# Optimization experiments

Measured on AMD Instinct MI355X. Metric: run time of the kernel, lower is better.

## Reference

```python
import jax, jax.numpy as jnp
import numpy as np

V, A, E, K, F = 50000, 1000, 100, 256, 8   # vocab, num_apis, embed_dim, num_kernel, feature_dim
B, S = 256, 512                             # batch, seq_len
KS = (2, 3, 4, 5)


def setup_inputs() -> dict:
    key = jax.random.key(0)
    ks = jax.random.split(key, 32)
    rn = lambda k, shape, s=0.05: jax.random.normal(k, shape, dtype=jnp.float32) * s
    inp = {}
    inp["text_ids"] = jax.random.randint(ks[0], (B, S), 0, V)
    inp["emb_table"] = rn(ks[1], (V, E), 1.0).at[0].set(0.0)  # padding_idx=0
    for i, h in enumerate(KS):
        inp[f"conv_w{h}"] = rn(ks[2 + 2 * i], (K, E, h))
        inp[f"conv_b{h}"] = rn(ks[3 + 2 * i], (K,))
    inp["sc_fcl_w"] = rn(ks[10], (A, 4 * K)); inp["sc_fcl_b"] = rn(ks[11], (A,))
    inp["fic_fc_w"] = rn(ks[12], (F, 4 * K)); inp["fic_fc_b"] = rn(ks[13], (F,))
    inp["api_emb"] = jax.random.uniform(ks[14], (F, A), dtype=jnp.float32)  # nn.Parameter(torch.rand)
    inp["mlp_w1"] = rn(ks[15], (F, 2 * F)); inp["mlp_b1"] = rn(ks[16], (F,))
    inp["mlp_w2"] = rn(ks[17], (1, F));     inp["mlp_b2"] = rn(ks[18], (1,))
    inp["fic_fcl_w"] = rn(ks[19], (A, 2 * A)); inp["fic_fcl_b"] = rn(ks[20], (A,))
    inp["fusion_w"] = rn(ks[21], (A, 2 * A)); inp["fusion_b"] = rn(ks[22], (A,))
    inp["out_w"] = rn(ks[23], (A, A)); inp["out_b"] = rn(ks[24], (A,))
    return inp


def reference(text_ids, emb_table, conv_w2, conv_b2, conv_w3, conv_b3,
              conv_w4, conv_b4, conv_w5, conv_b5, sc_fcl_w, sc_fcl_b,
              fic_fc_w, fic_fc_b, api_emb, mlp_w1, mlp_b1, mlp_w2, mlp_b2,
              fic_fcl_w, fic_fcl_b, fusion_w, fusion_b, out_w, out_b):
    # Embedding -> [B, E, S] (channels-first for Conv1d)
    x = emb_table[text_ids].transpose(0, 2, 1)
    pooled = []
    for w, b in ((conv_w2, conv_b2), (conv_w3, conv_b3), (conv_w4, conv_b4), (conv_w5, conv_b5)):
        y = jax.lax.conv_general_dilated(x, w, (1,), 'VALID',
                                         dimension_numbers=('NCH', 'OIH', 'NCH'))
        y = jax.nn.relu(y + b[None, :, None])
        pooled.append(jnp.max(y, axis=-1))            # AdaptiveMaxPool1d(1)
    e = jnp.concatenate(pooled, axis=1)               # [B, 4K]
    u_sc = e @ sc_fcl_w.T + sc_fcl_b                  # [B, A]
    u_t = e @ fic_fc_w.T + fic_fc_b                   # [B, F]
    u_mm = u_t @ api_emb                              # [B, A]
    # Fused broadcast-MLP replacing the per-sample Python loop:
    # cat([u_t repeated over A, api_emb.T]) @ W1.T == u_t@W1a.T (+) apiT@W1b.T
    w1a, w1b = mlp_w1[:, :F], mlp_w1[:, F:]
    z = (u_t @ w1a.T)[:, None, :] + (api_emb.T @ w1b.T)[None, :, :] + mlp_b1  # [B, A, F]
    u_mlp = jnp.tanh(jnp.einsum('baf,f->ba', z, mlp_w2[0]) + mlp_b2[0])       # [B, A]
    u_fic = jnp.tanh(jnp.concatenate([u_mm, u_mlp], axis=1) @ fic_fcl_w.T + fic_fcl_b)
    u_mmf = jnp.concatenate([u_sc, u_fic], axis=1) @ fusion_w.T + fusion_b    # dropout = identity (eval)
    return u_mmf @ out_w.T + out_b
```

## Files before the change

kernel.cpp:

```cpp
#include <hip/hip_runtime.h>
#include <hip/hip_bf16.h>
#include <math.h>


typedef __attribute__((ext_vector_type(8))) short short8;
typedef __attribute__((ext_vector_type(4))) short short4v;
typedef __attribute__((ext_vector_type(4))) float f32x4;

__device__ __forceinline__ void gld_lds16(const void* g, void* l) {
  __builtin_amdgcn_global_load_lds(
      (const __attribute__((address_space(1))) unsigned int*)g,
      (__attribute__((address_space(3))) unsigned int*)l, 16, 0, 0);
}

__device__ __forceinline__ short bf16of(float f) {
  union { float f; unsigned u; } x; x.f = f;
  unsigned r = (x.u + 0x7fff + ((x.u >> 16) & 1)) >> 16;
  return (short)r;
}

#define O1 6400128
#define O2 7055488
#define O3 8104064
#define O4 10201216
#define O5 12298368
#define O6 13346944
#define OT 13478024
__global__ __launch_bounds__(256) void prep_all(
    const int* __restrict__ text_ids, const float* __restrict__ emb,
    const float* __restrict__ w2, const float* __restrict__ w3,
    const float* __restrict__ w4, const float* __restrict__ w5,
    const float* __restrict__ b2, const float* __restrict__ b3,
    const float* __restrict__ b4, const float* __restrict__ b5,
    const float* __restrict__ sc_w, const float* __restrict__ fic_w,
    const float* __restrict__ fus_w, const float* __restrict__ out_w,
    __hip_bfloat16* __restrict__ emb_bf, __hip_bfloat16* __restrict__ Wc,
    float* __restrict__ cb, __hip_bfloat16* __restrict__ wt_sc,
    __hip_bfloat16* __restrict__ wt_fic, __hip_bfloat16* __restrict__ wt_fus,
    __hip_bfloat16* __restrict__ wt_out, int* __restrict__ ids_pad) {
  for (int v = blockIdx.x * 256 + threadIdx.x; v < OT / 4;
       v += gridDim.x * 256) {
    const int idx = v * 4;
    if (idx < O1) {
      const int row = idx >> 7, e = idx & 127;
      float4 f = make_float4(0.f, 0.f, 0.f, 0.f);
      if (row < 50000 && e < 100)
        f = *(const float4*)(emb + row * 100 + e);
      *(short4v*)(emb_bf + idx) =
          (short4v){bf16of(f.x), bf16of(f.y), bf16of(f.z), bf16of(f.w)};
    } else if (idx < O2) {
      const int t = idx - O1;
      const int n = t / 640, k = t % 640;
      const int h = 2 + (n >> 8), kc = n & 255;
      const int dh = k >> 7, e = k & 127;
      const float* w = (h == 2) ? w2 : (h == 3) ? w3 : (h == 4) ? w4 : w5;
      short4v o;
#pragma unroll
      for (int i = 0; i < 4; ++i)
        o[i] = (dh < h && e + i < 100) ? bf16of(w[(kc * 100 + e + i) * h + dh])
                                       : (short)0;
      *(short4v*)(Wc + t) = o;
      if (k == 0) {
        const float* bb = (h == 2) ? b2 : (h == 3) ? b3 : (h == 4) ? b4 : b5;
        cb[n] = bb[kc];
      }
    } else if (idx < O3) {
      const int t = idx - O2;
      const int n = t >> 10, k = t & 1023;
      float4 f = make_float4(0.f, 0.f, 0.f, 0.f);
      if (n < 1000) f = *(const float4*)(sc_w + n * 1024 + k);
      *(short4v*)(wt_sc + t) =
          (short4v){bf16of(f.x), bf16of(f.y), bf16of(f.z), bf16of(f.w)};
    } else if (idx < O4) {
      const int t = idx - O3;
      const int n = t >> 11, k = t & 2047;
      float4 f = make_float4(0.f, 0.f, 0.f, 0.f);
      if (n < 1000 && k < 2000) f = *(const float4*)(fic_w + n * 2000 + k);
      *(short4v*)(wt_fic + t) =
          (short4v){bf16of(f.x), bf16of(f.y), bf16of(f.z), bf16of(f.w)};
    } else if (idx < O5) {
      const int t = idx - O4;
      const int n = t >> 11, k = t & 2047;
      float4 f = make_float4(0.f, 0.f, 0.f, 0.f);
      if (n < 1000 && k < 2000) f = *(const float4*)(fus_w + n * 2000 + k);
      *(short4v*)(wt_fus + t) =
          (short4v){bf16of(f.x), bf16of(f.y), bf16of(f.z), bf16of(f.w)};
    } else if (idx < O6) {
      const int t = idx - O5;
      const int n = t >> 10, k = t & 1023;
      float4 f = make_float4(0.f, 0.f, 0.f, 0.f);
      if (n < 1000 && k < 1000) f = *(const float4*)(out_w + n * 1000 + k);
      *(short4v*)(wt_out + t) =
          (short4v){bf16of(f.x), bf16of(f.y), bf16of(f.z), bf16of(f.w)};
    } else {
      const int t = idx - O6;
      if (t + 3 < 131072) {
        *(int4*)(ids_pad + t) = *(const int4*)(text_ids + t);
      } else {
#pragma unroll
        for (int i = 0; i < 4; ++i)
          ids_pad[t + i] = (t + i < 131072) ? text_ids[t + i] : 50000;
      }
    }
  }
}

__global__ __launch_bounds__(256, 2) void conv_mfma(const __hip_bfloat16* __restrict__ Eb_,
                                                    const int* __restrict__ ids_pad,
                                                    const __hip_bfloat16* __restrict__ Wc_,
                                                    const float* __restrict__ cb,
                                                    float* __restrict__ e_out,
                                                    __hip_bfloat16* __restrict__ e_bf) {
  __shared__ __align__(16) short As[2][128 * 64];
  __shared__ __align__(16) short Bs[2][128 * 64];
  __shared__ int ids_s[520];
  __shared__ float pm_s[4][64];
  const int g = blockIdx.x;
  const int xcd = g & 7, i = g >> 3;
  const int nb = 7 - (i & 7);
  const int b = ((i >> 3) << 3) | xcd;
  const int N0 = nb << 7;
  const int h = 2 + (nb >> 1);
  const int nt = 2 * h;
  const int NS = 4 * nt;
  const int tid = threadIdx.x;
  const int lane = tid & 63;
  const int wid = tid >> 6;
  const int wr = wid >> 1, wc = wid & 1;
  const short* Eb = (const short*)Eb_;
  const short* Wc = (const short*)Wc_;

  ids_s[tid] = ids_pad[b * 512 + tid];
  ids_s[256 + tid] = ids_pad[b * 512 + 256 + tid];
  if (tid < 4) ids_s[512 + tid] = ids_pad[b * 512 + 512 + tid];
  __syncthreads();

  f32x4 acc[4][4];
#pragma unroll
  for (int ii = 0; ii < 4; ++ii)
#pragma unroll
    for (int jj = 0; jj < 4; ++jj) acc[ii][jj] = (f32x4){0.f, 0.f, 0.f, 0.f};
  float pm[4] = {-3.0e38f, -3.0e38f, -3.0e38f, -3.0e38f};

  int s_sub = 0, s_kk = 0;
  auto STAGE_NEXT = [&](int buf) {
    const int ms = s_sub << 7;
    const int k0 = s_kk << 6;
    const int dh = k0 >> 7, e0 = k0 & 127;
#pragma unroll
    for (int ii = 0; ii < 4; ++ii) {
      const int c = tid + (ii << 8);
      const int row = c >> 3, cs = c & 7;
      const int scs = cs ^ (row & 7);
      const int id = ids_s[ms + row + dh];
      gld_lds16(Eb + ((long)id << 7) + e0 + scs * 8, &As[buf][c * 8]);
      gld_lds16(Wc + (long)(N0 + row) * 640 + k0 + scs * 8, &Bs[buf][c * 8]);
    }
    if (++s_kk == nt) { s_kk = 0; ++s_sub; }
  };

  STAGE_NEXT(0);
  int c_kk = 0, c_sub = 0;
  for (int t = 0; t < NS; ++t) {
    if (t + 1 < NS) {
      STAGE_NEXT((t + 1) & 1);
      asm volatile("s_waitcnt vmcnt(8)" ::: "memory");
    } else {
      asm volatile("s_waitcnt vmcnt(0)" ::: "memory");
    }
    __builtin_amdgcn_s_barrier();
    const short* Ab = As[t & 1];
    const short* Bb = Bs[t & 1];
#pragma unroll
    for (int ks = 0; ks < 2; ++ks) {
      const int csq = ks * 4 + (lane >> 4);
      short8 av[4], bv[4];
#pragma unroll
      for (int mf = 0; mf < 4; ++mf) {
        const int row = wr * 64 + mf * 16 + (lane & 15);
        av[mf] = *(const short8*)&Ab[row * 64 + (csq ^ (row & 7)) * 8];
      }
#pragma unroll
      for (int nf = 0; nf < 4; ++nf) {
        const int row = wc * 64 + nf * 16 + (lane & 15);
        bv[nf] = *(const short8*)&Bb[row * 64 + (csq ^ (row & 7)) * 8];
      }
#pragma unroll
      for (int mf = 0; mf < 4; ++mf)
#pragma unroll
        for (int nf = 0; nf < 4; ++nf)
          acc[mf][nf] = __builtin_amdgcn_mfma_f32_16x16x32_bf16(av[mf], bv[nf], acc[mf][nf], 0, 0, 0);
    }
    if (++c_kk == nt) {
      c_kk = 0;
      const bool masked = (c_sub == 3);
#pragma unroll
      for (int nf = 0; nf < 4; ++nf) {
#pragma unroll
        for (int mf = 0; mf < 4; ++mf) {
          const int tloc = wr * 64 + mf * 16 + (lane >> 4) * 4;
#pragma unroll
          for (int r = 0; r < 4; ++r) {
            if (!masked || (tloc + r <= 128 - h))
              pm[nf] = fmaxf(pm[nf], acc[mf][nf][r]);
            acc[mf][nf][r] = 0.f;
          }
        }
      }
      ++c_sub;
    }
    asm volatile("s_waitcnt lgkmcnt(0)" ::: "memory");
    __builtin_amdgcn_s_barrier();
  }

#pragma unroll
  for (int nf = 0; nf < 4; ++nf) {
    float p = pm[nf];
    p = fmaxf(p, __shfl_xor(p, 16, 64));
    p = fmaxf(p, __shfl_xor(p, 32, 64));
    if ((lane >> 4) == 0) pm_s[wid][nf * 16 + (lane & 15)] = p;
  }
  __syncthreads();
  if (tid < 128) {
    const int wcx = tid >> 6, off = tid & 63;
    const int n = N0 + wcx * 64 + off;
    const float v0 = fmaxf(pm_s[wcx][off], pm_s[2 + wcx][off]);
    const float v = fmaxf(v0 + cb[n], 0.f);
    e_out[b * 1024 + n] = v;
    e_bf[b * 1024 + n] = __float2bfloat16(v);
  }
}

template<int ACT, int OUTBF>
__device__ __forceinline__ void gemm64_body(const short* __restrict__ A, int lda,
                                            const short* __restrict__ W, int ldw,
                                            const float* __restrict__ bias,
                                            void* __restrict__ Cv, int ldc,
                                            int N, int K, int cofs, int M0, int N0,
                                            short* As0, short* As1,
                                            short* Bs0, short* Bs1) {
  const int tid = threadIdx.x, lane = tid & 63;
  const int wid = tid >> 6;
  const int wr = wid >> 1, wc = wid & 1;
  short* Asb[2] = {As0, As1};
  short* Bsb[2] = {Bs0, Bs1};

  f32x4 acc[2][4];
#pragma unroll
  for (int i = 0; i < 2; ++i)
#pragma unroll
    for (int j = 0; j < 4; ++j) acc[i][j] = (f32x4){0.f, 0.f, 0.f, 0.f};

  auto STAGE = [&](int buf, int k0) {
#pragma unroll
    for (int i = 0; i < 2; ++i) {
      const int c = tid + (i << 8);
      const int row = c >> 3, cs = c & 7;
      const int scs = cs ^ (row & 7);
      gld_lds16(A + (long)(M0 + row) * lda + k0 + scs * 8, &Asb[buf][c * 8]);
    }
#pragma unroll
    for (int i = 0; i < 4; ++i) {
      const int c = tid + (i << 8);
      const int row = c >> 3, cs = c & 7;
      const int scs = cs ^ (row & 7);
      gld_lds16(W + (long)(N0 + row) * ldw + k0 + scs * 8, &Bsb[buf][c * 8]);
    }
  };

  const int nt = K >> 6;
  STAGE(0, 0);
  for (int t = 0; t < nt; ++t) {
    if (t + 1 < nt) {
      STAGE((t + 1) & 1, (t + 1) << 6);
      asm volatile("s_waitcnt vmcnt(6)" ::: "memory");
    } else {
      asm volatile("s_waitcnt vmcnt(0)" ::: "memory");
    }
    __builtin_amdgcn_s_barrier();
    const short* Ab = Asb[t & 1];
    const short* Bb = Bsb[t & 1];
#pragma unroll
    for (int ks = 0; ks < 2; ++ks) {
      const int csq = ks * 4 + (lane >> 4);
      short8 av[2], bv[4];
#pragma unroll
      for (int mf = 0; mf < 2; ++mf) {
        const int row = wr * 32 + mf * 16 + (lane & 15);
        av[mf] = *(const short8*)&Ab[row * 64 + (csq ^ (row & 7)) * 8];
      }
#pragma unroll
      for (int nf = 0; nf < 4; ++nf) {
        const int row = wc * 64 + nf * 16 + (lane & 15);
        bv[nf] = *(const short8*)&Bb[row * 64 + (csq ^ (row & 7)) * 8];
      }
#pragma unroll
      for (int mf = 0; mf < 2; ++mf)
#pragma unroll
        for (int nf = 0; nf < 4; ++nf)
          acc[mf][nf] = __builtin_amdgcn_mfma_f32_16x16x32_bf16(av[mf], bv[nf], acc[mf][nf], 0, 0, 0);
    }
    asm volatile("s_waitcnt lgkmcnt(0)" ::: "memory");
    __builtin_amdgcn_s_barrier();
  }

#pragma unroll
  for (int nf = 0; nf < 4; ++nf) {
    const int n = N0 + wc * 64 + nf * 16 + (lane & 15);
    const float bv = (n < N) ? bias[n] : 0.f;
#pragma unroll
    for (int mf = 0; mf < 2; ++mf) {
      const int m = M0 + wr * 32 + mf * 16 + (lane >> 4) * 4;
#pragma unroll
      for (int r = 0; r < 4; ++r) {
        float v = acc[mf][nf][r] + bv;
        if (ACT) v = tanhf(v);
        if (n < N) {
          if (OUTBF)
            ((__hip_bfloat16*)Cv)[(long)(m + r) * ldc + cofs + n] = __float2bfloat16(v);
          else
            ((float*)Cv)[(long)(m + r) * ldc + cofs + n] = v;
        }
      }
    }
  }
}

template<int ACT, int OUTBF>
__global__ __launch_bounds__(256) void gemm64(const __hip_bfloat16* __restrict__ A_,
                                              int lda,
                                              const __hip_bfloat16* __restrict__ W_,
                                              int ldw,
                                              const float* __restrict__ bias,
                                              void* __restrict__ Cv, int ldc,
                                              int N, int K) {
  __shared__ __align__(16) short As[2][64 * 64];
  __shared__ __align__(16) short Bs[2][128 * 64];
  gemm64_body<ACT, OUTBF>((const short*)A_, lda, (const short*)W_, ldw, bias,
                          Cv, ldc, N, K, 0, blockIdx.y << 6, blockIdx.x << 7,
                          As[0], As[1], Bs[0], Bs[1]);
}

__global__ __launch_bounds__(256) void gemm64_sc_fic(
    const __hip_bfloat16* __restrict__ e_bf,
    const __hip_bfloat16* __restrict__ cat_mm_bf,
    const __hip_bfloat16* __restrict__ wt_sc,
    const __hip_bfloat16* __restrict__ wt_fic,
    const float* __restrict__ sc_b, const float* __restrict__ fic_b,
    __hip_bfloat16* __restrict__ cat_sc) {
  __shared__ __align__(16) short As[2][64 * 64];
  __shared__ __align__(16) short Bs[2][128 * 64];
  const int z = blockIdx.z;
  if (z == 0)
    gemm64_body<0, 1>((const short*)e_bf, 1024, (const short*)wt_sc, 1024, sc_b,
                      cat_sc, 2048, 1000, 1024, 0, blockIdx.y << 6,
                      blockIdx.x << 7, As[0], As[1], Bs[0], Bs[1]);
  else
    gemm64_body<1, 1>((const short*)cat_mm_bf, 2048, (const short*)wt_fic, 2048,
                      fic_b, cat_sc, 2048, 1000, 2048, 1000, blockIdx.y << 6,
                      blockIdx.x << 7, As[0], As[1], Bs[0], Bs[1]);
}

__global__ __launch_bounds__(256) void k_heads(const float* __restrict__ e_buf,
                                               const float* __restrict__ W,
                                               const float* __restrict__ bias,
                                               const float* __restrict__ api,
                                               const float* __restrict__ mlp_w1,
                                               const float* __restrict__ mlp_b1,
                                               const float* __restrict__ mlp_w2,
                                               const float* __restrict__ mlp_b2,
                                               __hip_bfloat16* __restrict__ cat) {
  const int b = blockIdx.x, tid = threadIdx.x;
  float4 a = *(const float4*)(e_buf + b * 1024 + tid * 4);
  float acc[8];
#pragma unroll
  for (int f = 0; f < 8; ++f) {
    float4 w = *(const float4*)(W + f * 1024 + tid * 4);
    acc[f] = a.x * w.x + a.y * w.y + a.z * w.z + a.w * w.w;
  }
#pragma unroll
  for (int f = 0; f < 8; ++f)
    for (int off = 32; off; off >>= 1) acc[f] += __shfl_down(acc[f], off);
  __shared__ float red[4][8];
  __shared__ float ut_s[8];
  __shared__ float s1_s;
  if ((tid & 63) == 0) {
#pragma unroll
    for (int f = 0; f < 8; ++f) red[tid >> 6][f] = acc[f];
  }
  __syncthreads();
  if (tid == 0) {
    float s = 0.f;
#pragma unroll
    for (int f = 0; f < 8; ++f)
      ut_s[f] = red[0][f] + red[1][f] + red[2][f] + red[3][f] + bias[f];
#pragma unroll
    for (int f = 0; f < 8; ++f) {
      float t1 = 0.f;
#pragma unroll
      for (int fp = 0; fp < 8; ++fp) t1 += mlp_w1[f * 16 + fp] * ut_s[fp];
      s += t1 * mlp_w2[f];
    }
    s1_s = s;
  }
  __syncthreads();
  const float s1v = s1_s;
#pragma unroll
  for (int i = 0; i < 4; ++i) {
    const int j = tid + i * 256;
    if (j < 1000) {
      float ap[8];
#pragma unroll
      for (int fp = 0; fp < 8; ++fp) ap[fp] = api[fp * 1000 + j];
      float umm = 0.f;
#pragma unroll
      for (int f = 0; f < 8; ++f) umm += ut_s[f] * ap[f];
      float s2 = mlp_b2[0];
#pragma unroll
      for (int f = 0; f < 8; ++f) {
        float t2 = mlp_b1[f];
#pragma unroll
        for (int fp = 0; fp < 8; ++fp) t2 += mlp_w1[f * 16 + 8 + fp] * ap[fp];
        s2 += t2 * mlp_w2[f];
      }
      cat[b * 2048 + j] = __float2bfloat16(umm);
      cat[b * 2048 + 1000 + j] = __float2bfloat16(tanhf(s1v + s2));
    }
  }
  if (tid < 48) cat[b * 2048 + 2000 + tid] = __float2bfloat16(0.f);
}

__global__ __launch_bounds__(256) void transpose_w(const float* __restrict__ w,
                                                   float* __restrict__ wt, int EH) {
  int idx = blockIdx.x * 256 + threadIdx.x;
  if (idx >= 256 * EH) return;
  int k = idx / EH, r = idx % EH;
  wt[r * 256 + k] = w[idx];
}

template<int H>
__global__ __launch_bounds__(256) void conv_pool(const int* __restrict__ ids,
                                                 const float* __restrict__ emb,
                                                 const float* __restrict__ wt,
                                                 const float* __restrict__ cbias,
                                                 float* __restrict__ e_out,
                                                 int hidx) {
  const int b = blockIdx.y;
  const int t0 = blockIdx.x * 32;
  const int L = 512 - H + 1;
  __shared__ float4 xs4[100][10];
  float* xs = (float*)xs4;
  const int tid = threadIdx.x;
  const int WIN = 32 + H - 1;
  for (int idx = tid; idx < WIN * 25; idx += 256) {
    int p = idx / 25, c = idx % 25;
    int s = t0 + p;
    float4 v = make_float4(0.f, 0.f, 0.f, 0.f);
    if (s < 512) {
      int id = ids[b * 512 + s];
      v = *(const float4*)(emb + (long)id * 100 + c * 4);
    }
    xs[(4 * c + 0) * 40 + p] = v.x;
    xs[(4 * c + 1) * 40 + p] = v.y;
    xs[(4 * c + 2) * 40 + p] = v.z;
    xs[(4 * c + 3) * 40 + p] = v.w;
  }
  __syncthreads();
  const int k = tid;
  float acc[32];
#pragma unroll
  for (int t = 0; t < 32; ++t) acc[t] = 0.f;
  const float* wk = wt + k;
  for (int e = 0; e < 100; ++e) {
    float win[36];
#pragma unroll
    for (int i = 0; i < 9; ++i)
      *(float4*)&win[i * 4] = *(const float4*)&xs[e * 40 + i * 4];
    float wr[H];
#pragma unroll
    for (int dh = 0; dh < H; ++dh) wr[dh] = wk[(e * H + dh) * 256];
#pragma unroll
    for (int t = 0; t < 32; ++t) {
      float s = acc[t];
#pragma unroll
      for (int dh = 0; dh < H; ++dh) s = fmaf(wr[dh], win[t + dh], s);
      acc[t] = s;
    }
  }
  const float bk = cbias[k];
  float m = 0.f;
#pragma unroll
  for (int t = 0; t < 32; ++t) {
    if (t0 + t < L) m = fmaxf(m, fmaxf(acc[t] + bk, 0.f));
  }
  atomicMax((int*)&e_out[b * 1024 + hidx * 256 + k], __float_as_int(m));
}

__global__ __launch_bounds__(256) void k_ut_s1(const float* __restrict__ e_buf,
                                               const float* __restrict__ W,
                                               const float* __restrict__ bias,
                                               const float* __restrict__ mlp_w1,
                                               const float* __restrict__ mlp_w2,
                                               float* __restrict__ u_t,
                                               float* __restrict__ s1) {
  const int b = blockIdx.x, tid = threadIdx.x;
  float4 a = *(const float4*)(e_buf + b * 1024 + tid * 4);
  float acc[8];
#pragma unroll
  for (int f = 0; f < 8; ++f) {
    float4 w = *(const float4*)(W + f * 1024 + tid * 4);
    acc[f] = a.x * w.x + a.y * w.y + a.z * w.z + a.w * w.w;
  }
#pragma unroll
  for (int f = 0; f < 8; ++f)
    for (int off = 32; off; off >>= 1) acc[f] += __shfl_down(acc[f], off);
  __shared__ float red[4][8];
  if ((tid & 63) == 0) {
#pragma unroll
    for (int f = 0; f < 8; ++f) red[tid >> 6][f] = acc[f];
  }
  __syncthreads();
  if (tid == 0) {
    float ut[8];
#pragma unroll
    for (int f = 0; f < 8; ++f) {
      ut[f] = red[0][f] + red[1][f] + red[2][f] + red[3][f] + bias[f];
      u_t[b * 8 + f] = ut[f];
    }
    float s = 0.f;
#pragma unroll
    for (int f = 0; f < 8; ++f) {
      float t1 = 0.f;
#pragma unroll
      for (int fp = 0; fp < 8; ++fp) t1 += mlp_w1[f * 16 + fp] * ut[fp];
      s += t1 * mlp_w2[f];
    }
    s1[b] = s;
  }
}

__global__ __launch_bounds__(256) void k_s2(const float* __restrict__ api,
                                            const float* __restrict__ mlp_w1,
                                            const float* __restrict__ mlp_b1,
                                            const float* __restrict__ mlp_w2,
                                            const float* __restrict__ mlp_b2,
                                            float* __restrict__ s2) {
  int a = blockIdx.x * 256 + threadIdx.x;
  if (a >= 1000) return;
  float ap[8];
#pragma unroll
  for (int fp = 0; fp < 8; ++fp) ap[fp] = api[fp * 1000 + a];
  float s = mlp_b2[0];
#pragma unroll
  for (int f = 0; f < 8; ++f) {
    float t2 = mlp_b1[f];
#pragma unroll
    for (int fp = 0; fp < 8; ++fp) t2 += mlp_w1[f * 16 + 8 + fp] * ap[fp];
    s += t2 * mlp_w2[f];
  }
  s2[a] = s;
}

__global__ __launch_bounds__(256) void k_cat_f32(const float* __restrict__ u_t,
                                                 const float* __restrict__ api,
                                                 const float* __restrict__ s1,
                                                 const float* __restrict__ s2,
                                                 float* __restrict__ cat_mm) {
  int j = blockIdx.x * 256 + threadIdx.x;
  int b = blockIdx.y;
  if (j >= 2000) return;
  if (j < 1000) {
    float v = 0.f;
#pragma unroll
    for (int f = 0; f < 8; ++f) v += u_t[b * 8 + f] * api[f * 1000 + j];
    cat_mm[b * 2000 + j] = v;
  } else {
    cat_mm[b * 2000 + j] = tanhf(s1[b] + s2[j - 1000]);
  }
}

template<int ACT>
__global__ __launch_bounds__(256) void gemm_tn(const float* __restrict__ A, int lda,
                                               const float* __restrict__ W, int ldw,
                                               const float* __restrict__ bias,
                                               float* __restrict__ C, int ldc,
                                               int M, int N, int K) {
  __shared__ float As[8][33];
  __shared__ float Ws[8][33];
  const int n0 = blockIdx.x * 32, m0 = blockIdx.y * 32;
  const int tid = threadIdx.x;
  const int tx = tid % 16, ty = tid / 16;
  const int ms = tid / 8, ks = tid % 8;
  float acc[2][2] = {{0.f, 0.f}, {0.f, 0.f}};
  for (int k0 = 0; k0 < K; k0 += 8) {
    As[ks][ms] = A[(m0 + ms) * lda + k0 + ks];
    int n = n0 + ms;
    Ws[ks][ms] = (n < N) ? W[n * ldw + k0 + ks] : 0.f;
    __syncthreads();
#pragma unroll
    for (int kk = 0; kk < 8; ++kk) {
      float a0 = As[kk][ty], a1 = As[kk][ty + 16];
      float w0 = Ws[kk][tx], w1 = Ws[kk][tx + 16];
      acc[0][0] = fmaf(a0, w0, acc[0][0]);
      acc[0][1] = fmaf(a0, w1, acc[0][1]);
      acc[1][0] = fmaf(a1, w0, acc[1][0]);
      acc[1][1] = fmaf(a1, w1, acc[1][1]);
    }
    __syncthreads();
  }
#pragma unroll
  for (int i = 0; i < 2; ++i)
#pragma unroll
    for (int j = 0; j < 2; ++j) {
      int m = m0 + ty + 16 * i, n = n0 + tx + 16 * j;
      if (n < N) {
        float v = acc[i][j] + bias[n];
        if (ACT) v = tanhf(v);
        C[m * ldc + n] = v;
      }
    }
}

extern "C" void kernel_launch(void* const* d_in, const int* in_sizes, int n_in,
                              void* d_out, int out_size, void* d_ws, size_t ws_size,
                              hipStream_t stream) {
  const int*   text_ids  = (const int*)d_in[0];
  const float* emb       = (const float*)d_in[1];
  const float* cw2       = (const float*)d_in[2];
  const float* cb2       = (const float*)d_in[3];
  const float* cw3       = (const float*)d_in[4];
  const float* cb3       = (const float*)d_in[5];
  const float* cw4       = (const float*)d_in[6];
  const float* cb4       = (const float*)d_in[7];
  const float* cw5       = (const float*)d_in[8];
  const float* cb5       = (const float*)d_in[9];
  const float* sc_w      = (const float*)d_in[10];
  const float* sc_b      = (const float*)d_in[11];
  const float* fic_fc_w  = (const float*)d_in[12];
  const float* fic_fc_b  = (const float*)d_in[13];
  const float* api       = (const float*)d_in[14];
  const float* mlp_w1    = (const float*)d_in[15];
  const float* mlp_b1    = (const float*)d_in[16];
  const float* mlp_w2    = (const float*)d_in[17];
  const float* mlp_b2    = (const float*)d_in[18];
  const float* fic_fcl_w = (const float*)d_in[19];
  const float* fic_fcl_b = (const float*)d_in[20];
  const float* fusion_w  = (const float*)d_in[21];
  const float* fusion_b  = (const float*)d_in[22];
  const float* out_w     = (const float*)d_in[23];
  const float* out_b     = (const float*)d_in[24];

  float* ws = (float*)d_ws;
  float* e_buf = ws;
  float* cbias = e_buf + 262144;
  __hip_bfloat16* bfb       = (__hip_bfloat16*)(cbias + 1024);
  __hip_bfloat16* e_bf      = bfb;
  __hip_bfloat16* cat_mm_bf = e_bf + 262144;
  __hip_bfloat16* cat_sc_bf = cat_mm_bf + 524288;
  __hip_bfloat16* u_mmf_bf  = cat_sc_bf + 524288;
  __hip_bfloat16* emb_bf    = u_mmf_bf + 262144;
  __hip_bfloat16* Wc        = emb_bf + 6400128;
  __hip_bfloat16* wt_sc     = Wc + 655360;
  __hip_bfloat16* wt_fic    = wt_sc + 1048576;
  __hip_bfloat16* wt_fus    = wt_fic + 2097152;
  __hip_bfloat16* wt_out    = wt_fus + 2097152;
  int* ids_pad = (int*)(wt_out + 1048576);
  const size_t need_fast =
      263168UL * 4 + 14919808UL * 2 + 131080UL * 4;

  if (ws_size >= need_fast) {
    prep_all<<<4096, 256, 0, stream>>>(text_ids, emb, cw2, cw3, cw4, cw5,
                                       cb2, cb3, cb4, cb5, sc_w, fic_fcl_w,
                                       fusion_w, out_w, emb_bf, Wc, cbias,
                                       wt_sc, wt_fic, wt_fus, wt_out, ids_pad);
    conv_mfma<<<2048, 256, 0, stream>>>(emb_bf, ids_pad, Wc, cbias, e_buf, e_bf);
    k_heads<<<256, 256, 0, stream>>>(e_buf, fic_fc_w, fic_fc_b, api, mlp_w1,
                                     mlp_b1, mlp_w2, mlp_b2, cat_mm_bf);
    gemm64_sc_fic<<<dim3(8, 4, 2), 256, 0, stream>>>(e_bf, cat_mm_bf, wt_sc,
                                                     wt_fic, sc_b, fic_fcl_b,
                                                     cat_sc_bf);
    gemm64<0, 1><<<dim3(8, 4), 256, 0, stream>>>(cat_sc_bf, 2048, wt_fus, 2048,
                                                 fusion_b, u_mmf_bf, 1024,
                                                 1000, 2048);
    gemm64<0, 0><<<dim3(8, 4), 256, 0, stream>>>(u_mmf_bf, 1024, wt_out, 1024,
                                                 out_b, d_out, 1000, 1000, 1024);
  } else {
    hipMemsetAsync(e_buf, 0, 262144 * sizeof(float), stream);
    float* u_t    = (float*)bfb;
    float* s1     = u_t + 2048;
    float* s2     = s1 + 256;
    float* cat_mm = s2 + 1024;
    float* cat_sc = cat_mm + 512000;
    float* u_mmf  = cat_sc + 512000;
    float* wt     = u_mmf + 256000;
    transpose_w<<<200, 256, 0, stream>>>(cw2, wt + 0,      200);
    transpose_w<<<300, 256, 0, stream>>>(cw3, wt + 51200,  300);
    transpose_w<<<400, 256, 0, stream>>>(cw4, wt + 128000, 400);
    transpose_w<<<500, 256, 0, stream>>>(cw5, wt + 230400, 500);
    conv_pool<2><<<dim3(16, 256), 256, 0, stream>>>(text_ids, emb, wt + 0,      cb2, e_buf, 0);
    conv_pool<3><<<dim3(16, 256), 256, 0, stream>>>(text_ids, emb, wt + 51200,  cb3, e_buf, 1);
    conv_pool<4><<<dim3(16, 256), 256, 0, stream>>>(text_ids, emb, wt + 128000, cb4, e_buf, 2);
    conv_pool<5><<<dim3(16, 256), 256, 0, stream>>>(text_ids, emb, wt + 230400, cb5, e_buf, 3);
    k_ut_s1<<<256, 256, 0, stream>>>(e_buf, fic_fc_w, fic_fc_b, mlp_w1, mlp_w2, u_t, s1);
    k_s2<<<4, 256, 0, stream>>>(api, mlp_w1, mlp_b1, mlp_w2, mlp_b2, s2);
    k_cat_f32<<<dim3(8, 256), 256, 0, stream>>>(u_t, api, s1, s2, cat_mm);
    gemm_tn<0><<<dim3(32, 8), 256, 0, stream>>>(e_buf, 1024, sc_w, 1024, sc_b,
                                                cat_sc, 2000, 256, 1000, 1024);
    gemm_tn<1><<<dim3(32, 8), 256, 0, stream>>>(cat_mm, 2000, fic_fcl_w, 2000, fic_fcl_b,
                                                cat_sc + 1000, 2000, 256, 1000, 2000);
    gemm_tn<0><<<dim3(32, 8), 256, 0, stream>>>(cat_sc, 2000, fusion_w, 2000, fusion_b,
                                                u_mmf, 1000, 256, 1000, 2000);
    gemm_tn<0><<<dim3(32, 8), 256, 0, stream>>>(u_mmf, 1000, out_w, 1000, out_b,
                                                (float*)d_out, 1000, 256, 1000, 1000);
  }
}
```

Measured before the change: 256.4 us.

## Share weight tiles across two sequence subtiles in conv MFMA loop

Restructures the conv kernel's main loop so each pass processes two 128-row sequence subtiles against the same weight K-slice, with separate accumulator sets. Each weight tile is staged into LDS once per pair instead of once per subtile. The second subtile partly reuses the weight fragments already held in registers. This cuts global/LDS traffic for weights and some LDS reads, at the cost of doubling live accumulator registers under launch_bounds(256,2), which may cause spills or lower occupancy.

Measured after the change: 271.8 us. +6.0%, slower.

```diff
diff --git a/kernel.cpp b/kernel.cpp
--- a/kernel.cpp
+++ b/kernel.cpp
@@ -122,7 +122,6 @@
   const int N0 = nb << 7;
   const int h = 2 + (nb >> 1);
   const int nt = 2 * h;
-  const int NS = 4 * nt;
   const int tid = threadIdx.x;
   const int lane = tid & 63;
   const int wid = tid >> 6;
@@ -135,90 +134,137 @@
   if (tid < 4) ids_s[512 + tid] = ids_pad[b * 512 + 512 + tid];
   __syncthreads();
 
-  f32x4 acc[4][4];
-#pragma unroll
-  for (int ii = 0; ii < 4; ++ii)
-#pragma unroll
-    for (int jj = 0; jj < 4; ++jj) acc[ii][jj] = (f32x4){0.f, 0.f, 0.f, 0.f};
   float pm[4] = {-3.0e38f, -3.0e38f, -3.0e38f, -3.0e38f};
 
-  int s_sub = 0, s_kk = 0;
-  auto STAGE_NEXT = [&](int buf) {
-    const int ms = s_sub << 7;
-    const int k0 = s_kk << 6;
-    const int dh = k0 >> 7, e0 = k0 & 127;
-#pragma unroll
-    for (int ii = 0; ii < 4; ++ii) {
-      const int c = tid + (ii << 8);
-      const int row = c >> 3, cs = c & 7;
-      const int scs = cs ^ (row & 7);
-      const int id = ids_s[ms + row + dh];
-      gld_lds16(Eb + ((long)id << 7) + e0 + scs * 8, &As[buf][c * 8]);
-      gld_lds16(Wc + (long)(N0 + row) * 640 + k0 + scs * 8, &Bs[buf][c * 8]);
-    }
-    if (++s_kk == nt) { s_kk = 0; ++s_sub; }
+  auto FOLD = [&](f32x4 (&acc)[4][4], bool masked) {
+#pragma unroll
+    for (int nf = 0; nf < 4; ++nf) {
+#pragma unroll
+      for (int mf = 0; mf < 4; ++mf) {
+        const int tloc = wr * 64 + mf * 16 + (lane >> 4) * 4;
+#pragma unroll
+        for (int r = 0; r < 4; ++r) {
+          if (!masked || (tloc + r <= 128 - h))
+            pm[nf] = fmaxf(pm[nf], acc[mf][nf][r]);
+        }
+      }
+    }
   };
 
-  STAGE_NEXT(0);
-  int c_kk = 0, c_sub = 0;
-  for (int t = 0; t < NS; ++t) {
-    if (t + 1 < NS) {
-      STAGE_NEXT((t + 1) & 1);
-      asm volatile("s_waitcnt vmcnt(8)" ::: "memory");
-    } else {
-      asm volatile("s_waitcnt vmcnt(0)" ::: "memory");
-    }
-    __builtin_amdgcn_s_barrier();
-    const short* Ab = As[t & 1];
-    const short* Bb = Bs[t & 1];
-#pragma unroll
-    for (int ks = 0; ks < 2; ++ks) {
-      const int csq = ks * 4 + (lane >> 4);
-      short8 av[4], bv[4];
-#pragma unroll
-      for (int mf = 0; mf < 4; ++mf) {
-        const int row = wr * 64 + mf * 16 + (lane & 15);
-        av[mf] = *(const short8*)&Ab[row * 64 + (csq ^ (row & 7)) * 8];
-      }
-#pragma unroll
-      for (int nf = 0; nf < 4; ++nf) {
-        const int row = wc * 64 + nf * 16 + (lane & 15);
-        bv[nf] = *(const short8*)&Bb[row * 64 + (csq ^ (row & 7)) * 8];
-      }
-#pragma unroll
-      for (int mf = 0; mf < 4; ++mf)
-#pragma unroll
-        for (int nf = 0; nf < 4; ++nf)
-          acc[mf][nf] = __builtin_amdgcn_mfma_f32_16x16x32_bf16(av[mf], bv[nf], acc[mf][nf], 0, 0, 0);
-    }
-    if (++c_kk == nt) {
-      c_kk = 0;
-      const bool masked = (c_sub == 3);
-#pragma unroll
-      for (int nf = 0; nf < 4; ++nf) {
-#pragma unroll
-        for (int mf = 0; mf < 4; ++mf) {
-          const int tloc = wr * 64 + mf * 16 + (lane >> 4) * 4;
-#pragma unroll
-          for (int r = 0; r < 4; ++r) {
-            if (!masked || (tloc + r <= 128 - h))
-              pm[nf] = fmaxf(pm[nf], acc[mf][nf][r]);
-            acc[mf][nf][r] = 0.f;
+  for (int p = 0; p < 2; ++p) {
+    f32x4 accA[4][4], accB[4][4];
+#pragma unroll
+    for (int ii = 0; ii < 4; ++ii)
+#pragma unroll
+      for (int jj = 0; jj < 4; ++jj) {
+        accA[ii][jj] = (f32x4){0.f, 0.f, 0.f, 0.f};
+        accB[ii][jj] = (f32x4){0.f, 0.f, 0.f, 0.f};
+      }
+
+    auto STAGE_A = [&](int u) {
+      const int ms = ((p << 1) | (u & 1)) << 7;
+      const int kk = u >> 1;
+      const int k0 = kk << 6;
+      const int dh = k0 >> 7, e0 = k0 & 127;
+#pragma unroll
+      for (int ii = 0; ii < 4; ++ii) {
+        const int c = tid + (ii << 8);
+        const int row = c >> 3, cs = c & 7;
+        const int scs = cs ^ (row & 7);
+        const int id = ids_s[ms + row + dh];
+        gld_lds16(Eb + ((long)id << 7) + e0 + scs * 8, &As[u & 1][c * 8]);
+      }
+    };
+    auto STAGE_B = [&](int kk) {
+      const int k0 = kk << 6;
+#pragma unroll
+      for (int ii = 0; ii < 4; ++ii) {
+        const int c = tid + (ii << 8);
+        const int row = c >> 3, cs = c & 7;
+        const int scs = cs ^ (row & 7);
+        gld_lds16(Wc + (long)(N0 + row) * 640 + k0 + scs * 8, &Bs[kk & 1][c * 8]);
+      }
+    };
+
+    STAGE_A(0); STAGE_B(0);
+    const int NU = 2 * nt;
+    short8 bv[4];
+    for (int u = 0; u < NU; ++u) {
+      const int kk = u >> 1;
+      int issued = 0;
+      if (u + 1 < NU) { STAGE_A(u + 1); issued = 4; }
+      if ((u & 1) == 0 && kk + 1 < nt) { STAGE_B(kk + 1); issued += 4; }
+      if (issued == 8)      asm volatile("s_waitcnt vmcnt(8)" ::: "memory");
+      else if (issued == 4) asm volatile("s_waitcnt vmcnt(4)" ::: "memory");
+      else                  asm volatile("s_waitcnt vmcnt(0)" ::: "memory");
+      __builtin_amdgcn_s_barrier();
+      const short* Ab = As[u & 1];
+      const short* Bb = Bs[kk & 1];
+      if ((u & 1) == 0) {
+#pragma unroll
+        for (int ks = 0; ks < 2; ++ks) {
+          const int csq = ks * 4 + (lane >> 4);
+          short8 av[4];
+#pragma unroll
+          for (int mf = 0; mf < 4; ++mf) {
+            const int row = wr * 64 + mf * 16 + (lane & 15);
+            av[mf] = *(const short8*)&Ab[row * 64 + (csq ^ (row & 7)) * 8];
+          }
+#pragma unroll
+          for (int nf = 0; nf < 4; ++nf) {
+            const int row = wc * 64 + nf * 16 + (lane & 15);
+            bv[nf] = *(const short8*)&Bb[row * 64 + (csq ^ (row & 7)) * 8];
+          }
+#pragma unroll
+          for (int mf = 0; mf < 4; ++mf)
+#pragma unroll
+            for (int nf = 0; nf < 4; ++nf)
+              accA[mf][nf] = __builtin_amdgcn_mfma_f32_16x16x32_bf16(
+                  av[mf], bv[nf], accA[mf][nf], 0, 0, 0);
+          if (ks == 0) {
           }
         }
-      }
-      ++c_sub;
-    }
-    asm volatile("s_waitcnt lgkmcnt(0)" ::: "memory");
-    __builtin_amdgcn_s_barrier();
+      } else {
+#pragma unroll
+        for (int ks = 0; ks < 2; ++ks) {
+          const int csq = ks * 4 + (lane >> 4);
+          short8 av[4], bvl[4];
+#pragma unroll
+          for (int mf = 0; mf < 4; ++mf) {
+            const int row = wr * 64 + mf * 16 + (lane & 15);
+            av[mf] = *(const short8*)&Ab[row * 64 + (csq ^ (row & 7)) * 8];
+          }
+          if (ks == 1) {
+#pragma unroll
+            for (int nf = 0; nf < 4; ++nf) bvl[nf] = bv[nf];
+          } else {
+#pragma unroll
+            for (int nf = 0; nf < 4; ++nf) {
+              const int row = wc * 64 + nf * 16 + (lane & 15);
+              bvl[nf] = *(const short8*)&Bb[row * 64 + (csq ^ (row & 7)) * 8];
+            }
+          }
+#pragma unroll
+          for (int mf = 0; mf < 4; ++mf)
+#pragma unroll
+            for (int nf = 0; nf < 4; ++nf)
+              accB[mf][nf] = __builtin_amdgcn_mfma_f32_16x16x32_bf16(
+                  av[mf], bvl[nf], accB[mf][nf], 0, 0, 0);
+        }
+      }
+      asm volatile("s_waitcnt lgkmcnt(0)" ::: "memory");
+      __builtin_amdgcn_s_barrier();
+    }
+    FOLD(accA, false);
+    FOLD(accB, p == 1);
   }
 
 #pragma unroll
   for (int nf = 0; nf < 4; ++nf) {
-    float p = pm[nf];
-    p = fmaxf(p, __shfl_xor(p, 16, 64));
-    p = fmaxf(p, __shfl_xor(p, 32, 64));
-    if ((lane >> 4) == 0) pm_s[wid][nf * 16 + (lane & 15)] = p;
+    float pv = pm[nf];
+    pv = fmaxf(pv, __shfl_xor(pv, 16, 64));
+    pv = fmaxf(pv, __shfl_xor(pv, 32, 64));
+    if ((lane >> 4) == 0) pm_s[wid][nf * 16 + (lane & 15)] = pv;
   }
   __syncthreads();
   if (tid < 128) {
```
